# Optimization experiments

Hardware: AMD Instinct MI355X
Metric: run time of the kernel (lower is better)

## Reference

```python
import jax, jax.numpy as jnp
import numpy as np

KS = 3      # kernel size
PAD = 1     # zero padding
STRIDE = 1
N = KS * KS # 9 sampling points per pixel


def _deform_conv(feature, offset, weight):
    """DeformConv2d: bilinear sample at learned offsets then 3x3 conv (no bias)."""
    b, c, h, w = feature.shape
    x = jnp.pad(feature, ((0, 0), (0, 0), (PAD, PAD), (PAD, PAD)))
    hp, wp = h + 2 * PAD, w + 2 * PAD
    dt = feature.dtype
    # p_n: kernel grid offsets, x(rows) first then y(cols) -> (2N,)
    rng = jnp.arange(-(KS - 1) // 2, (KS - 1) // 2 + 1, dtype=dt)
    pn_x, pn_y = jnp.meshgrid(rng, rng, indexing='ij')
    # p_0: base sampling grid starting at 1 (accounts for zero padding)
    p0_x, p0_y = jnp.meshgrid(jnp.arange(1, h + 1, dtype=dt),
                              jnp.arange(1, w + 1, dtype=dt), indexing='ij')
    # sampling locations p = p_0 + p_n + offset, split into x/y -> (b,h,w,N)
    off = jnp.transpose(offset, (0, 2, 3, 1))  # (b,h,w,2N)
    px = p0_x[None, :, :, None] + pn_x.reshape(-1)[None, None, None, :] + off[..., :N]
    py = p0_y[None, :, :, None] + pn_y.reshape(-1)[None, None, None, :] + off[..., N:]
    q_lt_x = jnp.clip(jnp.floor(px), 0, hp - 1)
    q_lt_y = jnp.clip(jnp.floor(py), 0, wp - 1)
    q_rb_x = jnp.clip(jnp.floor(px) + 1, 0, hp - 1)
    q_rb_y = jnp.clip(jnp.floor(py) + 1, 0, wp - 1)
    px = jnp.clip(px, 0, hp - 1)
    py = jnp.clip(py, 0, wp - 1)
    # bilinear weights for the 4 corners
    g_lt = (1 + (q_lt_x - px)) * (1 + (q_lt_y - py))
    g_rb = (1 - (q_rb_x - px)) * (1 - (q_rb_y - py))
    g_lb = (1 + (q_lt_x - px)) * (1 - (q_rb_y - py))
    g_rt = (1 - (q_rb_x - px)) * (1 + (q_lt_y - py))
    x_flat = x.reshape(b, c, hp * wp)

    def gather(qx, qy):
        idx = (qx * wp + qy).astype(jnp.int32).reshape(b, 1, -1)
        v = jnp.take_along_axis(x_flat, jnp.broadcast_to(idx, (b, c, h * w * N)), axis=2)
        return v.reshape(b, c, h, w, N)

    x_off = (g_lt[:, None] * gather(q_lt_x, q_lt_y)
             + g_rb[:, None] * gather(q_rb_x, q_rb_y)
             + g_lb[:, None] * gather(q_lt_x, q_rb_y)
             + g_rt[:, None] * gather(q_rb_x, q_lt_y))  # (b,c,h,w,N)
    # equivalent of _reshape_x_offset + conv(ks, stride=ks)
    x_off = x_off.reshape(b, c, h, w, KS, KS)
    return jnp.einsum('bchwij,ocij->bohw', x_off, weight)


def setup_inputs() -> dict:
    key = jax.random.key(0)
    k1, k2, k3 = jax.random.split(key, 3)
    B, C, H, W = 4, 256, 64, 64
    feature = jax.random.normal(k1, (B, C, H, W), dtype=jnp.float32)
    offset = jax.random.normal(k2, (B, 2 * N, H, W), dtype=jnp.float32)
    weight = jax.random.normal(k3, (C, C, KS, KS), dtype=jnp.float32) / np.sqrt(C * N)
    return {"feature": feature, "offset": offset, "weight": weight}


def reference(feature, offset, weight):
    f1 = jax.nn.relu(_deform_conv(feature, offset, weight))
    return jax.nn.relu(f1 + feature)
```

## Files before the change

### kernel.cpp

```cpp
#include <hip/hip_runtime.h>

#define HW    4096
#define J_TOT 16384
#define K_TOT 2304
#define C_CH  256

typedef unsigned short u16;
typedef unsigned int   u32;
typedef __attribute__((ext_vector_type(8))) short short8;
typedef __attribute__((ext_vector_type(4))) float f32x4;
typedef __attribute__((ext_vector_type(8))) unsigned short us8;
typedef __attribute__((ext_vector_type(4))) unsigned short us4;

__device__ __forceinline__ float b2f(u16 u) { return __uint_as_float(((u32)u) << 16); }
__device__ __forceinline__ u16 f2b(float x) {
  u32 u = __float_as_uint(x);
  u += 0x7FFFu + ((u >> 16) & 1u);
  return (u16)(u >> 16);
}

__device__ __forceinline__ void gload_lds16(const u16* g, u16* l) {
  __builtin_amdgcn_global_load_lds(
      (__attribute__((address_space(1))) void*)(void*)g,
      (__attribute__((address_space(3))) void*)(void*)l, 16, 0, 0);
}

__global__ void k_detect(const u16* __restrict__ f, int* __restrict__ flag) {
  __shared__ int sh[256];
  int t = threadIdx.x;
  int hits = 0;
  for (int i = t; i < 2048; i += 256) {
    u16 u = f[2 * i];
    int e = (u >> 7) & 0xFF;
    hits += (e >= 100 && e <= 141) ? 1 : 0;
  }
  sh[t] = hits;
  __syncthreads();
  if (t == 0) {
    int s = 0;
    for (int i = 0; i < 256; i++) s += sh[i];
    flag[0] = (s > 1024) ? 1 : 0;
  }
}

__global__ void k_prep(const void* __restrict__ featv, u16* __restrict__ ftr,
                       const void* __restrict__ wv, u16* __restrict__ Wr,
                       const int* __restrict__ flag) {
  int isbf = *flag;
  int tx = threadIdx.x;
  int ty = threadIdx.y;
  int z = blockIdx.z;
  if (z < 4) {
    __shared__ u16 tile[32][33];
    int b = z;
    int hw0 = blockIdx.x << 5;
    int c0 = blockIdx.y << 5;
    if (isbf) {
      const u16* f = (const u16*)featv;
#pragma unroll
      for (int i = 0; i < 4; i++) {
        int c = c0 + ty + i * 8;
        tile[ty + i * 8][tx] = f[(((size_t)(b * C_CH + c)) << 12) + hw0 + tx];
      }
    } else {
      const float* f = (const float*)featv;
#pragma unroll
      for (int i = 0; i < 4; i++) {
        int c = c0 + ty + i * 8;
        tile[ty + i * 8][tx] = f2b(f[(((size_t)(b * C_CH + c)) << 12) + hw0 + tx]);
      }
    }
    __syncthreads();
#pragma unroll
    for (int i = 0; i < 4; i++) {
      int hw = hw0 + ty + i * 8;
      ftr[(((size_t)(b * HW + hw)) << 8) + c0 + tx] = tile[tx][ty + i * 8];
    }
  } else {
    int bid = blockIdx.x + (blockIdx.y << 7);
    int flat = ty * 32 + tx;
    for (int idx = bid * 256 + flat; idx < C_CH * K_TOT; idx += 1024 * 256) {
      int c = idx & 255;
      int n = (idx >> 8) % 9;
      int o = idx / K_TOT;
      int src = (o * 256 + c) * 9 + n;
      if (isbf) Wr[idx] = ((const u16*)wv)[src];
      else      Wr[idx] = f2b(((const float*)wv)[src]);
    }
  }
}

#define NT 36

#define A_DMA(bufi)                                                          \
  do {                                                                       \
    gload_lds16(asrc0, &As[bufi][wave * 1024]);                              \
    gload_lds16(asrc1, &As[bufi][wave * 1024 + 512]);                        \
    asrc0 += 64; asrc1 += 64;                                                \
  } while (0)

#define PLOAD(tile)                                                          \
  do {                                                                       \
    int np = (tile) >> 2, c0 = ((tile) & 3) << 6;                            \
    w0 = gs[np][0][pp]; w1 = gs[np][1][pp];                                  \
    w2 = gs[np][2][pp]; w3 = gs[np][3][pp];                                  \
    q0 = *(const us4*)(ftr + isx[np][0][pp] + c0 + cb4);                     \
    q1 = *(const us4*)(ftr + isx[np][1][pp] + c0 + cb4);                     \
    q2 = *(const us4*)(ftr + isx[np][2][pp] + c0 + cb4);                     \
    q3 = *(const us4*)(ftr + isx[np][3][pp] + c0 + cb4);                     \
  } while (0)

#define PFIN(bufi)                                                           \
  do {                                                                       \
    us4 ov;                                                                  \
    _Pragma("unroll")                                                        \
    for (int i = 0; i < 4; i++) {                                            \
      float v = w0 * b2f(q0[i]) + w1 * b2f(q1[i]) +                          \
                w2 * b2f(q2[i]) + w3 * b2f(q3[i]);                           \
      ov[i] = f2b(v);                                                        \
    }                                                                        \
    *(us4*)(&Bs[bufi][bofs]) = ov;                                           \
  } while (0)

#define GEMM_COMPUTE(bufi)                                                   \
  do {                                                                       \
    short8 af[2][2], bf[2][2];                                               \
    _Pragma("unroll")                                                        \
    for (int kk = 0; kk < 2; kk++) {                                         \
      int go = (((kk << 2) + lk) ^ swz) << 3;                                \
      _Pragma("unroll")                                                      \
      for (int oi = 0; oi < 2; oi++)                                         \
        af[oi][kk] = *(const short8*)(As[bufi] + (wo * 32 + oi * 16 + lr) * 64 + go); \
      _Pragma("unroll")                                                      \
      for (int ji = 0; ji < 2; ji++)                                         \
        bf[ji][kk] = *(const short8*)(Bs[bufi] + (wj * 32 + ji * 16 + lr) * 64 + go); \
    }                                                                        \
    __builtin_amdgcn_s_setprio(1);                                           \
    _Pragma("unroll")                                                        \
    for (int kk = 0; kk < 2; kk++)                                           \
      _Pragma("unroll")                                                      \
      for (int oi = 0; oi < 2; oi++)                                         \
        _Pragma("unroll")                                                    \
        for (int ji = 0; ji < 2; ji++)                                       \
          acc[oi][ji] = __builtin_amdgcn_mfma_f32_16x16x32_bf16(             \
              af[oi][kk], bf[ji][kk], acc[oi][ji], 0, 0, 0);                 \
    __builtin_amdgcn_s_setprio(0);                                           \
  } while (0)

__global__ __launch_bounds__(1024, 4) void k_gemm(const u16* __restrict__ Wr,
                                                  const u16* __restrict__ ftr,
                                                  const void* __restrict__ offv,
                                                  const void* __restrict__ featv,
                                                  void* __restrict__ outv,
                                                  const int* __restrict__ flag) {
  __shared__ u16 As[2][256 * 64];
  __shared__ u16 Bs[2][64 * 64];
  __shared__ float gs[9][4][64];
  __shared__ int   isx[9][4][64];
  int isbf = *flag;
  int j0 = blockIdx.x << 6;
  int b = j0 >> 12;
  int hw0 = j0 & (HW - 1);
  int t = threadIdx.x;
  int wave = t >> 6, lane = t & 63;
  int wj = wave >> 3, wo = wave & 7;
  int lr = lane & 15, lk = lane >> 4;
  int swz = lr & 7;

  if (t < 576) {
    int n = t >> 6, p = t & 63;
    int hw = hw0 + p;
    int h = hw >> 6, w = hw & 63;
    size_t obi = (((size_t)(b * 18 + n)) << 12) + hw;
    float ox, oy;
    if (isbf) {
      const u16* po = (const u16*)offv;
      ox = b2f(po[obi]);
      oy = b2f(po[obi + (9u << 12)]);
    } else {
      const float* po = (const float*)offv;
      ox = po[obi];
      oy = po[obi + (9u << 12)];
    }
    int ki = n / 3, kj = n % 3;
    float px = (float)(h + ki) + ox;
    float py = (float)(w + kj) + oy;
    float fx = floorf(px), fy = floorf(py);
    float qltx = fminf(fmaxf(fx, 0.f), 65.f);
    float qlty = fminf(fmaxf(fy, 0.f), 65.f);
    float qrbx = fminf(fmaxf(fx + 1.f, 0.f), 65.f);
    float qrby = fminf(fmaxf(fy + 1.f, 0.f), 65.f);
    float pcx = fminf(fmaxf(px, 0.f), 65.f);
    float pcy = fminf(fmaxf(py, 0.f), 65.f);
    float dltx = 1.f + (qltx - pcx);
    float drbx = 1.f - (qrbx - pcx);
    float dlty = 1.f + (qlty - pcy);
    float drby = 1.f - (qrby - pcy);
    float g0 = dltx * dlty;
    float g1 = drbx * drby;
    float g2 = dltx * drby;
    float g3 = drbx * dlty;
    int x0 = (int)qltx, y0 = (int)qlty, x1 = (int)qrbx, y1 = (int)qrby;
    int v0 = (x0 >= 1 && x0 <= 64 && y0 >= 1 && y0 <= 64);
    int v1 = (x1 >= 1 && x1 <= 64 && y1 >= 1 && y1 <= 64);
    int v2 = (x0 >= 1 && x0 <= 64 && y1 >= 1 && y1 <= 64);
    int v3 = (x1 >= 1 && x1 <= 64 && y0 >= 1 && y0 <= 64);
    int base = b << 12;
    isx[n][0][p] = v0 ? ((base + ((x0 - 1) << 6) + (y0 - 1)) << 8) : 0;
    isx[n][1][p] = v1 ? ((base + ((x1 - 1) << 6) + (y1 - 1)) << 8) : 0;
    isx[n][2][p] = v2 ? ((base + ((x0 - 1) << 6) + (y1 - 1)) << 8) : 0;
    isx[n][3][p] = v3 ? ((base + ((x1 - 1) << 6) + (y0 - 1)) << 8) : 0;
    gs[n][0][p] = v0 ? g0 : 0.f;
    gs[n][1][p] = v1 ? g1 : 0.f;
    gs[n][2][p] = v2 ? g2 : 0.f;
    gs[n][3][p] = v3 ? g3 : 0.f;
  }

  f32x4 acc[2][2];
  f32x4 zero = {0.f, 0.f, 0.f, 0.f};
#pragma unroll
  for (int i = 0; i < 2; i++)
#pragma unroll
    for (int j = 0; j < 2; j++) acc[i][j] = zero;

  int rb = lane >> 3;
  int cs = ((lane & 7) ^ rb) << 3;
  const u16* asrc0 = Wr + (size_t)(wave * 16 + 0 + rb) * K_TOT + cs;
  const u16* asrc1 = Wr + (size_t)(wave * 16 + 8 + rb) * K_TOT + cs;

  int pp = t >> 4, qq = t & 15;
  int cgp = qq >> 1, half = qq & 1;
  int bofs = pp * 64 + ((cgp ^ (pp & 7)) << 3) + (half << 2);
  int cb4 = (cgp << 3) + (half << 2);

  __syncthreads();

  us4 q0, q1, q2, q3;
  float w0, w1, w2, w3;

  PLOAD(0);
  A_DMA(0);
  PFIN(0);
  __syncthreads();

  for (int tt = 0; tt < NT - 1; ++tt) {
    int cbuf = tt & 1, nbuf = cbuf ^ 1;
    PLOAD(tt + 1);
    A_DMA(nbuf);
    GEMM_COMPUTE(cbuf);
    PFIN(nbuf);
    __syncthreads();
  }
  GEMM_COMPUTE((NT - 1) & 1);

  int lq = lane >> 4;
#pragma unroll
  for (int oi = 0; oi < 2; oi++) {
#pragma unroll
    for (int ji = 0; ji < 2; ji++) {
      int j = j0 + wj * 32 + ji * 16 + lr;
      int bb_ = j >> 12, hw = j & (HW - 1);
      int o0 = wo * 32 + oi * 16 + lq * 4;
#pragma unroll
      for (int r = 0; r < 4; r++) {
        size_t oidx = (((size_t)(bb_ * C_CH + o0 + r)) << 12) + hw;
        float v = acc[oi][ji][r];
        v = fmaxf(v, 0.f);
        float ft = isbf ? b2f(((const u16*)featv)[oidx]) : ((const float*)featv)[oidx];
        v = fmaxf(v + ft, 0.f);
        if (isbf) ((u16*)outv)[oidx] = f2b(v);
        else      ((float*)outv)[oidx] = v;
      }
    }
  }
}

extern "C" void kernel_launch(void* const* d_in, const int* in_sizes, int n_in,
                              void* d_out, int out_size, void* d_ws, size_t ws_size,
                              hipStream_t stream) {
  const void* feat = d_in[0];
  const void* offs = d_in[1];
  const void* wght = d_in[2];

  const size_t off_flag = 0;
  const size_t off_wr   = 256;
  const size_t off_ftr  = off_wr + (size_t)1179648;
  const size_t need     = off_ftr + (size_t)8388608;
  if (ws_size < need) return;

  char* ws = (char*)d_ws;
  int* flag = (int*)(ws + off_flag);
  u16* Wr   = (u16*)(ws + off_wr);
  u16* ftr  = (u16*)(ws + off_ftr);

  k_detect<<<1, 256, 0, stream>>>((const u16*)feat, flag);
  k_prep<<<dim3(128, 8, 5), dim3(32, 8), 0, stream>>>(feat, ftr, wght, Wr, flag);
  k_gemm<<<J_TOT / 64, 1024, 0, stream>>>(Wr, ftr, offs, feat, d_out, flag);
}
```

Before: 136.1 us.

## Triple-buffer LDS tiles and prefetch two stages ahead with partial vmcnt waits

```diff
diff --git a/kernel.cpp b/kernel.cpp
--- a/kernel.cpp
+++ b/kernel.cpp
@@ -9,7 +9,6 @@
 typedef unsigned int   u32;
 typedef __attribute__((ext_vector_type(8))) short short8;
 typedef __attribute__((ext_vector_type(4))) float f32x4;
-typedef __attribute__((ext_vector_type(8))) unsigned short us8;
 typedef __attribute__((ext_vector_type(4))) unsigned short us4;
 
 __device__ __forceinline__ float b2f(u16 u) { return __uint_as_float(((u32)u) << 16); }
@@ -92,37 +91,43 @@
 
 #define NT 36
 
-#define A_DMA(bufi)                                                          \
-  do {                                                                       \
-    gload_lds16(asrc0, &As[bufi][wave * 1024]);                              \
-    gload_lds16(asrc1, &As[bufi][wave * 1024 + 512]);                        \
+#define A_DMA(Ab)                                                            \
+  do {                                                                       \
+    gload_lds16(asrc0, (Ab) + wave * 1024);                                  \
+    gload_lds16(asrc1, (Ab) + wave * 1024 + 512);                            \
     asrc0 += 64; asrc1 += 64;                                                \
   } while (0)
 
-#define PLOAD(tile)                                                          \
-  do {                                                                       \
-    int np = (tile) >> 2, c0 = ((tile) & 3) << 6;                            \
-    w0 = gs[np][0][pp]; w1 = gs[np][1][pp];                                  \
-    w2 = gs[np][2][pp]; w3 = gs[np][3][pp];                                  \
-    q0 = *(const us4*)(ftr + isx[np][0][pp] + c0 + cb4);                     \
-    q1 = *(const us4*)(ftr + isx[np][1][pp] + c0 + cb4);                     \
-    q2 = *(const us4*)(ftr + isx[np][2][pp] + c0 + cb4);                     \
-    q3 = *(const us4*)(ftr + isx[np][3][pp] + c0 + cb4);                     \
-  } while (0)
-
-#define PFIN(bufi)                                                           \
+#define PLOAD_S(tile, P)                                                     \
+  do {                                                                       \
+    if (((tile) & 3) == 0) {                                                 \
+      int np_ = (tile) >> 2;                                                 \
+      tw0 = gs[np_][0][pp]; tw1 = gs[np_][1][pp];                            \
+      tw2 = gs[np_][2][pp]; tw3 = gs[np_][3][pp];                            \
+      ti0 = isx[np_][0][pp]; ti1 = isx[np_][1][pp];                          \
+      ti2 = isx[np_][2][pp]; ti3 = isx[np_][3][pp];                          \
+    }                                                                        \
+    int c0_ = (((tile) & 3) << 6) + cb4;                                     \
+    P##w0 = tw0; P##w1 = tw1; P##w2 = tw2; P##w3 = tw3;                      \
+    P##q0 = *(const us4*)(ftr + ti0 + c0_);                                  \
+    P##q1 = *(const us4*)(ftr + ti1 + c0_);                                  \
+    P##q2 = *(const us4*)(ftr + ti2 + c0_);                                  \
+    P##q3 = *(const us4*)(ftr + ti3 + c0_);                                  \
+  } while (0)
+
+#define PFIN_S(P, Bb)                                                        \
   do {                                                                       \
     us4 ov;                                                                  \
     _Pragma("unroll")                                                        \
     for (int i = 0; i < 4; i++) {                                            \
-      float v = w0 * b2f(q0[i]) + w1 * b2f(q1[i]) +                          \
-                w2 * b2f(q2[i]) + w3 * b2f(q3[i]);                           \
+      float v = P##w0 * b2f(P##q0[i]) + P##w1 * b2f(P##q1[i]) +              \
+                P##w2 * b2f(P##q2[i]) + P##w3 * b2f(P##q3[i]);               \
       ov[i] = f2b(v);                                                        \
     }                                                                        \
-    *(us4*)(&Bs[bufi][bofs]) = ov;                                           \
-  } while (0)
-
-#define GEMM_COMPUTE(bufi)                                                   \
+    *(us4*)((Bb) + bofs) = ov;                                               \
+  } while (0)
+
+#define GEMM_COMPUTE(Ab, Bb)                                                 \
   do {                                                                       \
     short8 af[2][2], bf[2][2];                                               \
     _Pragma("unroll")                                                        \
@@ -130,10 +135,10 @@
       int go = (((kk << 2) + lk) ^ swz) << 3;                                \
       _Pragma("unroll")                                                      \
       for (int oi = 0; oi < 2; oi++)                                         \
-        af[oi][kk] = *(const short8*)(As[bufi] + (wo * 32 + oi * 16 + lr) * 64 + go); \
+        af[oi][kk] = *(const short8*)((Ab) + (wo * 32 + oi * 16 + lr) * 64 + go); \
       _Pragma("unroll")                                                      \
       for (int ji = 0; ji < 2; ji++)                                         \
-        bf[ji][kk] = *(const short8*)(Bs[bufi] + (wj * 32 + ji * 16 + lr) * 64 + go); \
+        bf[ji][kk] = *(const short8*)((Bb) + (wj * 32 + ji * 16 + lr) * 64 + go); \
     }                                                                        \
     __builtin_amdgcn_s_setprio(1);                                           \
     _Pragma("unroll")                                                        \
@@ -147,17 +152,30 @@
     __builtin_amdgcn_s_setprio(0);                                           \
   } while (0)
 
+#define CBAR()                                                               \
+  do {                                                                       \
+    asm volatile("s_waitcnt vmcnt(6) lgkmcnt(0)" ::: "memory");              \
+    __builtin_amdgcn_s_barrier();                                            \
+  } while (0)
+
+#define ROTATE()                                                             \
+  do {                                                                       \
+    u16* tp_ = Ac; Ac = An; An = Af; Af = tp_;                               \
+    tp_ = Bc; Bc = Bn; Bn = Bf; Bf = tp_;                                    \
+  } while (0)
+
 __global__ __launch_bounds__(1024, 4) void k_gemm(const u16* __restrict__ Wr,
                                                   const u16* __restrict__ ftr,
                                                   const void* __restrict__ offv,
                                                   const void* __restrict__ featv,
                                                   void* __restrict__ outv,
                                                   const int* __restrict__ flag) {
-  __shared__ u16 As[2][256 * 64];
-  __shared__ u16 Bs[2][64 * 64];
+  __shared__ u16 As[3][256 * 64];
+  __shared__ u16 Bs[3][64 * 64];
   __shared__ float gs[9][4][64];
   __shared__ int   isx[9][4][64];
   int isbf = *flag;
+  asm volatile("" :: "s"(isbf));
   int j0 = blockIdx.x << 6;
   int b = j0 >> 12;
   int hw0 = j0 & (HW - 1);
@@ -233,25 +251,41 @@
   int bofs = pp * 64 + ((cgp ^ (pp & 7)) << 3) + (half << 2);
   int cb4 = (cgp << 3) + (half << 2);
 
+  u16 *Ac = &As[0][0], *An = &As[1][0], *Af = &As[2][0];
+  u16 *Bc = &Bs[0][0], *Bn = &Bs[1][0], *Bf = &Bs[2][0];
+
   __syncthreads();
 
-  us4 q0, q1, q2, q3;
-  float w0, w1, w2, w3;
-
-  PLOAD(0);
-  A_DMA(0);
-  PFIN(0);
-  __syncthreads();
-
-  for (int tt = 0; tt < NT - 1; ++tt) {
-    int cbuf = tt & 1, nbuf = cbuf ^ 1;
-    PLOAD(tt + 1);
-    A_DMA(nbuf);
-    GEMM_COMPUTE(cbuf);
-    PFIN(nbuf);
-    __syncthreads();
-  }
-  GEMM_COMPUTE((NT - 1) & 1);
+  us4 aq0, aq1, aq2, aq3, bq0, bq1, bq2, bq3;
+  float aw0, aw1, aw2, aw3, bw0, bw1, bw2, bw3;
+  float tw0, tw1, tw2, tw3;
+  int ti0, ti1, ti2, ti3;
+
+  PLOAD_S(0, a); A_DMA(Ac);
+  PFIN_S(a, Bc);
+  PLOAD_S(1, b); A_DMA(An);
+  CBAR();
+
+#pragma unroll 1
+  for (int it = 0; it < 17; ++it) {
+    PLOAD_S(2 * it + 2, a);
+    A_DMA(Af);
+    GEMM_COMPUTE(Ac, Bc);
+    PFIN_S(b, Bn);
+    CBAR();
+    ROTATE();
+    PLOAD_S(2 * it + 3, b);
+    A_DMA(Af);
+    GEMM_COMPUTE(Ac, Bc);
+    PFIN_S(a, Bn);
+    CBAR();
+    ROTATE();
+  }
+  GEMM_COMPUTE(Ac, Bc);
+  PFIN_S(b, Bn);
+  asm volatile("s_waitcnt vmcnt(0) lgkmcnt(0)" ::: "memory");
+  __builtin_amdgcn_s_barrier();
+  GEMM_COMPUTE(An, Bn);
 
   int lq = lane >> 4;
 #pragma unroll
```

New measurement: 128.0 us. 1.06x faster.
